# Optimization experiments

Hardware: AMD Instinct MI355X
Metric: run time of the kernel (lower is better)

Reference implementation:

```python
import jax, jax.numpy as jnp
import numpy as np

N_NODES = 100000
MAX_DEG = 16
D_IN = 256
D_OUT = 256


def setup_inputs() -> dict:
    key = jax.random.key(0)
    k1, k2, k3, k4, k5 = jax.random.split(key, 5)
    x = jax.random.normal(k1, (N_NODES, D_IN), dtype=jnp.float32)
    # padded edge list: -1 marks padding; first column always valid so degree >= 1
    col0 = jax.random.randint(k2, (N_NODES, 1), 0, N_NODES)
    rest = jax.random.randint(k3, (N_NODES, MAX_DEG - 1), -1, N_NODES)
    edge_index = jnp.concatenate([col0, rest], axis=1).astype(jnp.int64)
    # torch Linear(2*D_IN, D_OUT): weight [D_OUT, 2*D_IN], bias [D_OUT]
    W = jax.random.normal(k4, (D_OUT, 2 * D_IN), dtype=jnp.float32) * 0.05
    b = jax.random.normal(k5, (D_OUT,), dtype=jnp.float32) * 0.05
    return {"x": x, "edge_index": edge_index, "W": W, "b": b}


def reference(x, edge_index, W, b):
    # pad with a zero row so index -1 (padding) gathers zeros, matching torch
    padded = jnp.concatenate([x, jnp.zeros((1, x.shape[1]), dtype=x.dtype)], axis=0)
    neigh = padded[edge_index]  # [N, MAX_DEG, D_IN]
    degree = jnp.sum(edge_index >= 0, axis=-1, keepdims=True).astype(x.dtype)  # [N, 1]
    neigh_agg = jnp.sum(neigh, axis=1) / degree  # mean aggregation, [N, D_IN]
    h = jnp.concatenate([x, neigh_agg], axis=1)  # [N, 2*D_IN]
    return h @ W.T + b
```

## Files before the change

kernel.cpp:

```cpp
#include <hip/hip_runtime.h>
#include <stdint.h>


#define MAX_DEG 16
#define D_IN 256
#define D_K 512
#define D_OUT 256
#define BM 16
#define LDS_STRIDE 520
#define N_NODES_C 100000

typedef __attribute__((ext_vector_type(8))) short bf16x8;
typedef __attribute__((ext_vector_type(4))) float f32x4;

__device__ __forceinline__ uint32_t f2bf(float f) {
    union { float f; uint32_t u; } v; v.f = f;
    uint32_t u = v.u;
    return (u + 0x7FFFu + ((u >> 16) & 1u)) >> 16;
}
__device__ __forceinline__ uint32_t pack2(float lo, float hi) {
    return f2bf(lo) | (f2bf(hi) << 16);
}

__global__ __launch_bounds__(256) void cast_all_kernel(
    const float* __restrict__ x, const float* __restrict__ W,
    ushort* __restrict__ Xb, ushort* __restrict__ Wb)
{
    const int b = blockIdx.x;
    const int tid = threadIdx.x;
    if (b < 12500) {
        const size_t i = (size_t)b * 2048 + tid * 8;
        float4 v0 = *(const float4*)(x + i);
        float4 v1 = *(const float4*)(x + i + 4);
        uint4 p = { pack2(v0.x, v0.y), pack2(v0.z, v0.w),
                    pack2(v1.x, v1.y), pack2(v1.z, v1.w) };
        *(uint4*)(Xb + i) = p;
    } else if (b == 12500) {
        if (tid < 32) {
            uint4 z = {0u, 0u, 0u, 0u};
            *(uint4*)(Xb + (size_t)N_NODES_C * D_IN + tid * 8) = z;
        }
    } else {
        const size_t i = (size_t)(b - 12501) * 2048 + tid * 8;
        float4 v0 = *(const float4*)(W + i);
        float4 v1 = *(const float4*)(W + i + 4);
        uint4 p = { pack2(v0.x, v0.y), pack2(v0.z, v0.w),
                    pack2(v1.x, v1.y), pack2(v1.z, v1.w) };
        *(uint4*)(Wb + i) = p;
    }
}

__global__ __launch_bounds__(256, 6) void sage_bf16_kernel(
    const ushort* __restrict__ Xb,
    const int* __restrict__ edge,
    const ushort* __restrict__ Wb,
    const float* __restrict__ bias,
    float* __restrict__ out)
{
    __shared__ ushort sH[BM * LDS_STRIDE];

    const int tid = threadIdx.x;
    const int node0 = blockIdx.x * BM;

    {
        const int m = tid >> 4;
        const int l = tid & 15;
        const int node = node0 + m;

        const uint4* xr = (const uint4*)(Xb + (size_t)node * D_IN + l * 16);
        uint4 s0 = xr[0], s1 = xr[1];
        uint4* dst = (uint4*)(sH + m * LDS_STRIDE + l * 16);
        dst[0] = s0; dst[1] = s1;

        const int4* ep = (const int4*)(edge + (size_t)node * MAX_DEG);
        int idx[16]; int deg = 0;
        #pragma unroll
        for (int g = 0; g < 4; ++g) {
            int4 e = ep[g];
            int v0 = e.x, v1 = e.y, v2 = e.z, v3 = e.w;
            deg += (v0 >= 0) + (v1 >= 0) + (v2 >= 0) + (v3 >= 0);
            idx[g*4+0] = v0 < 0 ? N_NODES_C : v0;
            idx[g*4+1] = v1 < 0 ? N_NODES_C : v1;
            idx[g*4+2] = v2 < 0 ? N_NODES_C : v2;
            idx[g*4+3] = v3 < 0 ? N_NODES_C : v3;
        }

        float c[16];
        #pragma unroll
        for (int q = 0; q < 16; ++q) c[q] = 0.f;

        #pragma unroll 4
        for (int d = 0; d < MAX_DEG; ++d) {
            const uint4* nr = (const uint4*)(Xb + (size_t)idx[d] * D_IN + l * 16);
            uint4 a0 = nr[0], a1 = nr[1];
            uint32_t u[8] = {a0.x, a0.y, a0.z, a0.w, a1.x, a1.y, a1.z, a1.w};
            #pragma unroll
            for (int q = 0; q < 8; ++q) {
                union { uint32_t ui; float f; } lo, hi;
                lo.ui = u[q] << 16;
                hi.ui = u[q] & 0xFFFF0000u;
                c[2*q]   += lo.f;
                c[2*q+1] += hi.f;
            }
        }

        const float inv = 1.0f / (float)deg;
        uint4 p0 = { pack2(c[0]*inv,  c[1]*inv),  pack2(c[2]*inv,  c[3]*inv),
                     pack2(c[4]*inv,  c[5]*inv),  pack2(c[6]*inv,  c[7]*inv) };
        uint4 p1 = { pack2(c[8]*inv,  c[9]*inv),  pack2(c[10]*inv, c[11]*inv),
                     pack2(c[12]*inv, c[13]*inv), pack2(c[14]*inv, c[15]*inv) };
        uint4* dst2 = (uint4*)(sH + m * LDS_STRIDE + D_IN + l * 16);
        dst2[0] = p0; dst2[1] = p1;
    }
    __syncthreads();

    {
        const int wave = tid >> 6;
        const int lane = tid & 63;
        const int quad = lane >> 4;
        const int r16  = lane & 15;

        f32x4 acc[4];
        #pragma unroll
        for (int j = 0; j < 4; ++j) {
            float bv = bias[wave * 64 + j * 16 + r16];
            acc[j] = (f32x4){bv, bv, bv, bv};
        }

        const ushort* arow = sH + r16 * LDS_STRIDE + quad * 8;
        #pragma unroll
        for (int ks = 0; ks < D_K / 32; ++ks) {
            bf16x8 a = *(const bf16x8*)(arow + ks * 32);
            #pragma unroll
            for (int j = 0; j < 4; ++j) {
                const int o = wave * 64 + j * 16 + r16;
                bf16x8 b = *(const bf16x8*)(Wb + (size_t)o * D_K + ks * 32 + quad * 8);
                acc[j] = __builtin_amdgcn_mfma_f32_16x16x32_bf16(a, b, acc[j], 0, 0, 0);
            }
        }

        #pragma unroll
        for (int j = 0; j < 4; ++j) {
            const int o = wave * 64 + j * 16 + r16;
            #pragma unroll
            for (int r = 0; r < 4; ++r) {
                const int row = node0 + quad * 4 + r;
                out[(size_t)row * D_OUT + o] = acc[j][r];
            }
        }
    }
}

__global__ __launch_bounds__(256) void cast_w_kernel(const float* __restrict__ W,
                                                     ushort* __restrict__ Wb) {
    int i = (blockIdx.x * 256 + threadIdx.x) * 4;
    float4 v = *(const float4*)(W + i);
    ushort4 p = { (ushort)f2bf(v.x), (ushort)f2bf(v.y),
                  (ushort)f2bf(v.z), (ushort)f2bf(v.w) };
    *(ushort4*)(Wb + i) = p;
}

__global__ __launch_bounds__(256) void sage_fp32_kernel(
    const float* __restrict__ x, const int* __restrict__ edge,
    const ushort* __restrict__ Wb, const float* __restrict__ bias,
    float* __restrict__ out)
{
    __shared__ ushort sH[32 * LDS_STRIDE];
    const int tid = threadIdx.x;
    const int node0 = blockIdx.x * 32;
    {
        const int m = tid >> 3, l = tid & 7;
        const int node = node0 + m;
        const float4* xrow = (const float4*)(x + (size_t)node * D_IN);
        ushort* dst = sH + m * LDS_STRIDE + l * 32;
        #pragma unroll
        for (int q = 0; q < 8; ++q) {
            float4 v = xrow[l * 8 + q];
            ushort4 p = { (ushort)f2bf(v.x), (ushort)f2bf(v.y),
                          (ushort)f2bf(v.z), (ushort)f2bf(v.w) };
            *(ushort4*)(dst + q * 4) = p;
        }
        float4 agg[8];
        #pragma unroll
        for (int q = 0; q < 8; ++q) agg[q] = make_float4(0.f,0.f,0.f,0.f);
        int deg = 0;
        for (int d = 0; d < MAX_DEG; ++d) {
            int nb = edge[(size_t)node * MAX_DEG + d];
            if (nb >= 0) {
                ++deg;
                const float4* nr = (const float4*)(x + (size_t)nb * D_IN);
                #pragma unroll
                for (int q = 0; q < 8; ++q) {
                    float4 t = nr[l * 8 + q];
                    agg[q].x += t.x; agg[q].y += t.y;
                    agg[q].z += t.z; agg[q].w += t.w;
                }
            }
        }
        const float inv = 1.0f / (float)deg;
        ushort* dst2 = sH + m * LDS_STRIDE + D_IN + l * 32;
        #pragma unroll
        for (int q = 0; q < 8; ++q) {
            ushort4 p = { (ushort)f2bf(agg[q].x*inv), (ushort)f2bf(agg[q].y*inv),
                          (ushort)f2bf(agg[q].z*inv), (ushort)f2bf(agg[q].w*inv) };
            *(ushort4*)(dst2 + q * 4) = p;
        }
    }
    __syncthreads();
    {
        const int wave = tid >> 6, lane = tid & 63;
        const int quad = lane >> 4, r16 = lane & 15;
        const int mt = wave & 1, nh = wave >> 1;
        f32x4 acc[8];
        #pragma unroll
        for (int j = 0; j < 8; ++j) {
            float bv = bias[(nh * 8 + j) * 16 + r16];
            acc[j] = (f32x4){bv, bv, bv, bv};
        }
        const ushort* arow = sH + (mt * 16 + r16) * LDS_STRIDE + quad * 8;
        #pragma unroll
        for (int ks = 0; ks < D_K / 32; ++ks) {
            bf16x8 a = *(const bf16x8*)(arow + ks * 32);
            #pragma unroll
            for (int j = 0; j < 8; ++j) {
                const int o = (nh * 8 + j) * 16 + r16;
                bf16x8 b = *(const bf16x8*)(Wb + (size_t)o * D_K + ks * 32 + quad * 8);
                acc[j] = __builtin_amdgcn_mfma_f32_16x16x32_bf16(a, b, acc[j], 0, 0, 0);
            }
        }
        #pragma unroll
        for (int j = 0; j < 8; ++j) {
            const int o = (nh * 8 + j) * 16 + r16;
            #pragma unroll
            for (int r = 0; r < 4; ++r) {
                const int row = node0 + mt * 16 + quad * 4 + r;
                out[(size_t)row * D_OUT + o] = acc[j][r];
            }
        }
    }
}

extern "C" void kernel_launch(void* const* d_in, const int* in_sizes, int n_in,
                              void* d_out, int out_size, void* d_ws, size_t ws_size,
                              hipStream_t stream) {
    const float* x    = (const float*)d_in[0];
    const int*   edge = (const int*)d_in[1];
    const float* W    = (const float*)d_in[2];
    const float* bias = (const float*)d_in[3];
    float* out = (float*)d_out;

    const size_t xb_bytes = (size_t)(N_NODES_C + 1) * D_IN * 2;
    const size_t wb_bytes = (size_t)D_OUT * D_K * 2;
    const int n = in_sizes[0] / D_IN;

    if (ws_size >= xb_bytes + wb_bytes) {
        ushort* Xb = (ushort*)d_ws;
        ushort* Wb = (ushort*)((char*)d_ws + xb_bytes);
        cast_all_kernel<<<12565, 256, 0, stream>>>(x, W, Xb, Wb);
        sage_bf16_kernel<<<n / BM, 256, 0, stream>>>(Xb, edge, Wb, bias, out);
    } else {
        ushort* Wb = (ushort*)d_ws;
        cast_w_kernel<<<(D_OUT * D_K) / 1024, 256, 0, stream>>>(W, Wb);
        sage_fp32_kernel<<<n / 32, 256, 0, stream>>>(x, edge, Wb, bias, out);
    }
}
```

Measured before the change: 418.7 us.

## Double node tile, batch neighbor gathers, and reuse W fragments across two M tiles

Raises the per-block node tile from 16 to 32 with 512 threads. The neighbor gather is split into two column halves, and all 16 neighbor rows are loaded up front so more memory requests are in flight. Lane addressing changes so that 16 lanes read one contiguous 256-byte segment. In the MFMA stage each wave computes a 32x32 output tile, so each W fragment loaded from global memory feeds two MFMAs and W traffic per node is halved. The cost is higher register pressure from the 16 staged uint4 loads and fewer resident blocks.

```diff
diff --git a/kernel.cpp b/kernel.cpp
--- a/kernel.cpp
+++ b/kernel.cpp
@@ -6,7 +6,7 @@
 #define D_IN 256
 #define D_K 512
 #define D_OUT 256
-#define BM 16
+#define BM 32
 #define LDS_STRIDE 520
 #define N_NODES_C 100000
 
@@ -50,7 +50,7 @@
     }
 }
 
-__global__ __launch_bounds__(256, 6) void sage_bf16_kernel(
+__global__ __launch_bounds__(512, 4) void sage_bf16_kernel(
     const ushort* __restrict__ Xb,
     const int* __restrict__ edge,
     const ushort* __restrict__ Wb,
@@ -67,85 +67,94 @@
         const int l = tid & 15;
         const int node = node0 + m;
 
-        const uint4* xr = (const uint4*)(Xb + (size_t)node * D_IN + l * 16);
-        uint4 s0 = xr[0], s1 = xr[1];
-        uint4* dst = (uint4*)(sH + m * LDS_STRIDE + l * 16);
-        dst[0] = s0; dst[1] = s1;
+        const uint4* xr = (const uint4*)(Xb + (size_t)node * D_IN);
+        uint4* selfdst = (uint4*)(sH + (size_t)m * LDS_STRIDE);
+        uint4 s0 = xr[l], s1 = xr[16 + l];
+        selfdst[l] = s0; selfdst[16 + l] = s1;
 
         const int4* ep = (const int4*)(edge + (size_t)node * MAX_DEG);
-        int idx[16]; int deg = 0;
+        uint32_t off[MAX_DEG]; int deg = 0;
         #pragma unroll
         for (int g = 0; g < 4; ++g) {
             int4 e = ep[g];
-            int v0 = e.x, v1 = e.y, v2 = e.z, v3 = e.w;
-            deg += (v0 >= 0) + (v1 >= 0) + (v2 >= 0) + (v3 >= 0);
-            idx[g*4+0] = v0 < 0 ? N_NODES_C : v0;
-            idx[g*4+1] = v1 < 0 ? N_NODES_C : v1;
-            idx[g*4+2] = v2 < 0 ? N_NODES_C : v2;
-            idx[g*4+3] = v3 < 0 ? N_NODES_C : v3;
-        }
-
-        float c[16];
-        #pragma unroll
-        for (int q = 0; q < 16; ++q) c[q] = 0.f;
-
-        #pragma unroll 4
-        for (int d = 0; d < MAX_DEG; ++d) {
-            const uint4* nr = (const uint4*)(Xb + (size_t)idx[d] * D_IN + l * 16);
-            uint4 a0 = nr[0], a1 = nr[1];
-            uint32_t u[8] = {a0.x, a0.y, a0.z, a0.w, a1.x, a1.y, a1.z, a1.w};
-            #pragma unroll
-            for (int q = 0; q < 8; ++q) {
-                union { uint32_t ui; float f; } lo, hi;
-                lo.ui = u[q] << 16;
-                hi.ui = u[q] & 0xFFFF0000u;
-                c[2*q]   += lo.f;
-                c[2*q+1] += hi.f;
-            }
-        }
-
+            deg += (e.x >= 0) + (e.y >= 0) + (e.z >= 0) + (e.w >= 0);
+            off[g*4+0] = (uint32_t)(e.x < 0 ? N_NODES_C : e.x) * 512u;
+            off[g*4+1] = (uint32_t)(e.y < 0 ? N_NODES_C : e.y) * 512u;
+            off[g*4+2] = (uint32_t)(e.z < 0 ? N_NODES_C : e.z) * 512u;
+            off[g*4+3] = (uint32_t)(e.w < 0 ? N_NODES_C : e.w) * 512u;
+        }
         const float inv = 1.0f / (float)deg;
-        uint4 p0 = { pack2(c[0]*inv,  c[1]*inv),  pack2(c[2]*inv,  c[3]*inv),
-                     pack2(c[4]*inv,  c[5]*inv),  pack2(c[6]*inv,  c[7]*inv) };
-        uint4 p1 = { pack2(c[8]*inv,  c[9]*inv),  pack2(c[10]*inv, c[11]*inv),
-                     pack2(c[12]*inv, c[13]*inv), pack2(c[14]*inv, c[15]*inv) };
-        uint4* dst2 = (uint4*)(sH + m * LDS_STRIDE + D_IN + l * 16);
-        dst2[0] = p0; dst2[1] = p1;
+        const char* xb = (const char*)Xb;
+
+        #pragma unroll 1
+        for (int c = 0; c < 2; ++c) {
+            const uint32_t coff = (uint32_t)(c * 256 + l * 16);
+            uint4 st[MAX_DEG];
+            #pragma unroll
+            for (int d = 0; d < MAX_DEG; ++d)
+                st[d] = *(const uint4*)(xb + (size_t)(off[d] + coff));
+
+            float a[8];
+            #pragma unroll
+            for (int q = 0; q < 8; ++q) a[q] = 0.f;
+            #pragma unroll
+            for (int d = 0; d < MAX_DEG; ++d) {
+                uint32_t u[4] = { st[d].x, st[d].y, st[d].z, st[d].w };
+                #pragma unroll
+                for (int q = 0; q < 4; ++q) {
+                    union { uint32_t ui; float f; } lo, hi;
+                    lo.ui = u[q] << 16;
+                    hi.ui = u[q] & 0xFFFF0000u;
+                    a[2*q]   += lo.f;
+                    a[2*q+1] += hi.f;
+                }
+            }
+            uint4 p = { pack2(a[0]*inv, a[1]*inv), pack2(a[2]*inv, a[3]*inv),
+                        pack2(a[4]*inv, a[5]*inv), pack2(a[6]*inv, a[7]*inv) };
+            *(uint4*)(sH + (size_t)m * LDS_STRIDE + D_IN + c * 128 + l * 8) = p;
+        }
     }
     __syncthreads();
 
     {
-        const int wave = tid >> 6;
+        const int w = tid >> 6;
         const int lane = tid & 63;
         const int quad = lane >> 4;
         const int r16  = lane & 15;
 
-        f32x4 acc[4];
-        #pragma unroll
-        for (int j = 0; j < 4; ++j) {
-            float bv = bias[wave * 64 + j * 16 + r16];
-            acc[j] = (f32x4){bv, bv, bv, bv};
-        }
-
-        const ushort* arow = sH + r16 * LDS_STRIDE + quad * 8;
+        f32x4 acc[2][2];
+        #pragma unroll
+        for (int j = 0; j < 2; ++j) {
+            float bv = bias[w * 32 + j * 16 + r16];
+            acc[0][j] = (f32x4){bv, bv, bv, bv};
+            acc[1][j] = (f32x4){bv, bv, bv, bv};
+        }
+
+        const ushort* a0p = sH + (size_t)r16 * LDS_STRIDE + quad * 8;
+        const ushort* a1p = a0p + 16 * LDS_STRIDE;
         #pragma unroll
         for (int ks = 0; ks < D_K / 32; ++ks) {
-            bf16x8 a = *(const bf16x8*)(arow + ks * 32);
-            #pragma unroll
-            for (int j = 0; j < 4; ++j) {
-                const int o = wave * 64 + j * 16 + r16;
+            bf16x8 a0 = *(const bf16x8*)(a0p + ks * 32);
+            bf16x8 a1 = *(const bf16x8*)(a1p + ks * 32);
+            #pragma unroll
+            for (int j = 0; j < 2; ++j) {
+                const int o = w * 32 + j * 16 + r16;
                 bf16x8 b = *(const bf16x8*)(Wb + (size_t)o * D_K + ks * 32 + quad * 8);
-                acc[j] = __builtin_amdgcn_mfma_f32_16x16x32_bf16(a, b, acc[j], 0, 0, 0);
-            }
-        }
-
-        #pragma unroll
-        for (int j = 0; j < 4; ++j) {
-            const int o = wave * 64 + j * 16 + r16;
-            #pragma unroll
-            for (int r = 0; r < 4; ++r) {
-                const int row = node0 + quad * 4 + r;
-                out[(size_t)row * D_OUT + o] = acc[j][r];
+                acc[0][j] = __builtin_amdgcn_mfma_f32_16x16x32_bf16(a0, b, acc[0][j], 0, 0, 0);
+                acc[1][j] = __builtin_amdgcn_mfma_f32_16x16x32_bf16(a1, b, acc[1][j], 0, 0, 0);
+            }
+        }
+
+        #pragma unroll
+        for (int mt = 0; mt < 2; ++mt) {
+            #pragma unroll
+            for (int j = 0; j < 2; ++j) {
+                const int o = w * 32 + j * 16 + r16;
+                #pragma unroll
+                for (int r = 0; r < 4; ++r) {
+                    const int row = node0 + mt * 16 + quad * 4 + r;
+                    out[(size_t)row * D_OUT + o] = acc[mt][j][r];
+                }
             }
         }
     }
@@ -257,7 +266,7 @@
         ushort* Xb = (ushort*)d_ws;
         ushort* Wb = (ushort*)((char*)d_ws + xb_bytes);
         cast_all_kernel<<<12565, 256, 0, stream>>>(x, W, Xb, Wb);
-        sage_bf16_kernel<<<n / BM, 256, 0, stream>>>(Xb, edge, Wb, bias, out);
+        sage_bf16_kernel<<<n / BM, 512, 0, stream>>>(Xb, edge, Wb, bias, out);
     } else {
         ushort* Wb = (ushort*)d_ws;
         cast_w_kernel<<<(D_OUT * D_K) / 1024, 256, 0, stream>>>(W, Wb);
```

Measured after the change: 364.8 us. -12.9%, faster.
